# Kernel tuning notes

Measured on AMD Instinct MI355X. Metric: run time of the kernel, lower is better.

## Reference

```python
import jax, jax.numpy as jnp
import numpy as np

N = 8192
F_IN = 128
D = 128
NEG_SLOPE = 0.2  # cfg.negativeslope (standard GAT value)
MASK_FILL = -9e15


def setup_inputs() -> dict:
    key = jax.random.key(0)
    k1, k2, k3, k4 = jax.random.split(key, 4)
    A = jax.random.randint(k1, (N, N), 0, 2, dtype=jnp.int32)
    X = jax.random.normal(k2, (N, F_IN), dtype=jnp.float32)
    # glorot init for Ws, xavier_uniform(gain=1.414) for a
    lim_w = float(np.sqrt(6.0 / (F_IN + D)))
    Ws = jax.random.uniform(k3, (F_IN, D), minval=-lim_w, maxval=lim_w, dtype=jnp.float32)
    lim_a = 1.414 * float(np.sqrt(6.0 / (2 * D + 1)))
    a = jax.random.uniform(k4, (2 * D, 1), minval=-lim_a, maxval=lim_a, dtype=jnp.float32)
    return {"A": A, "X": X, "Ws": Ws, "a": a}


def reference(A, X, Ws, a):
    # Wh: [N, D]
    Wh = X @ Ws
    d = Wh.shape[-1]
    # additive attention: e_ij = leaky_relu(Wh_i . a1 + Wh_j . a2)
    e1 = Wh @ a[:d]          # [N, 1]
    e2 = Wh @ a[d:]          # [N, 1]
    e = jax.nn.leaky_relu(e1 + e2.T, negative_slope=NEG_SLOPE)  # [N, N]
    e = jnp.where(A > 0, e, MASK_FILL)
    attn = jax.nn.softmax(e, axis=1)  # row-wise over neighbors
    H = attn @ Wh            # [N, D]
    return H
```

## Files before the change

kernel.cpp:

```cpp
#include <hip/hip_runtime.h>
#include <hip/hip_bf16.h>

#define NN 8192
#define DD 128

typedef __attribute__((ext_vector_type(8))) short short8;
typedef __attribute__((ext_vector_type(4))) float f32x4;
typedef __attribute__((ext_vector_type(4))) int i32x4;
typedef unsigned int u32;
typedef unsigned long long u64;

__device__ __forceinline__ ushort f2bf(float f) {
    __hip_bfloat16 h = __float2bfloat16(f);
    return *(ushort*)&h;
}

__device__ __forceinline__ void async_ld16(const void* g, void* l) {
    __builtin_amdgcn_global_load_lds(
        (const __attribute__((address_space(1))) u32*)g,
        (__attribute__((address_space(3))) u32*)l, 16, 0, 0);
}

#define PACK4(b, v, sh)                                     \
    b |= (u32)((v).x & 1) << (sh);                          \
    b |= (u32)((v).y & 1) << ((sh) + 1);                    \
    b |= (u32)((v).z & 1) << ((sh) + 2);                    \
    b |= (u32)((v).w & 1) << ((sh) + 3);

__global__ __launch_bounds__(256) void k3a_pack(const int* __restrict__ A,
                                                uint4* __restrict__ Ap) {
    u32 T = blockIdx.x * 256 + threadIdx.x;
    u32 row = T >> 6, q = T & 63, kb = q >> 2, kg = q & 3;
    const int* base = A + (size_t)row * NN + kb * 512 + kg * 8;
    u32 d[4];
#pragma unroll
    for (int h = 0; h < 2; ++h) {
        i32x4 v[16];
#pragma unroll
        for (int j = 0; j < 8; ++j) {
            int kt = h * 4 + (j >> 1), tp = j & 1;
            const int* p = base + kt * 64 + tp * 32;
            v[j * 2]     = __builtin_nontemporal_load((const i32x4*)p);
            v[j * 2 + 1] = __builtin_nontemporal_load((const i32x4*)(p + 4));
        }
        u32 b01 = 0, b23 = 0;
#pragma unroll
        for (int j = 0; j < 8; ++j) {
            u32 b = 0;
            PACK4(b, v[j * 2], 0);
            PACK4(b, v[j * 2 + 1], 4);
            if (j < 4) b01 |= b << (8 * j);
            else       b23 |= b << (8 * (j - 4));
        }
        d[h * 2] = b01; d[h * 2 + 1] = b23;
    }
    Ap[T] = make_uint4(d[0], d[1], d[2], d[3]);
}

__global__ __launch_bounds__(256) void k12_gemm(const float* __restrict__ X,
                                                const float* __restrict__ Ws,
                                                const float* __restrict__ a,
                                                ushort* __restrict__ WhT,
                                                float* __restrict__ C1,
                                                float* __restrict__ C1s,
                                                float2* __restrict__ E2) {
    __shared__ float lWs[128 * 132];
    __shared__ float lX[32 * 132];
    __shared__ ushort lT2[128 * 32];
    __shared__ float la[256];
    int t = threadIdx.x, bx = blockIdx.x;
    la[t] = a[t];
    const float4* Ws4 = (const float4*)Ws;
    const float4* X4 = (const float4*)X;
    for (int j = 0; j < 16; ++j) {
        int u = j * 256 + t;
        int k = u >> 5, c4 = u & 31;
        *(float4*)&lWs[k * 132 + c4 * 4] = Ws4[u];
    }
    for (int j = 0; j < 4; ++j) {
        int u = j * 256 + t;
        int r = u >> 5, c4 = u & 31;
        *(float4*)&lX[r * 132 + c4 * 4] = X4[bx * 1024 + u];
    }
    __syncthreads();
    int r0 = (t >> 5) * 4, c0 = (t & 31) * 4;
    float acc[4][4];
#pragma unroll
    for (int i = 0; i < 4; ++i)
#pragma unroll
        for (int j = 0; j < 4; ++j) acc[i][j] = 0.f;
#pragma unroll 4
    for (int k = 0; k < 128; ++k) {
        float4 wv = *(const float4*)&lWs[k * 132 + c0];
        float x0 = lX[(r0 + 0) * 132 + k];
        float x1 = lX[(r0 + 1) * 132 + k];
        float x2 = lX[(r0 + 2) * 132 + k];
        float x3 = lX[(r0 + 3) * 132 + k];
#pragma unroll
        for (int j = 0; j < 4; ++j) {
            acc[0][j] += x0 * ((const float*)&wv)[j];
            acc[1][j] += x1 * ((const float*)&wv)[j];
            acc[2][j] += x2 * ((const float*)&wv)[j];
            acc[3][j] += x3 * ((const float*)&wv)[j];
        }
    }
#pragma unroll
    for (int i = 0; i < 4; ++i)
#pragma unroll
        for (int j = 0; j < 4; ++j)
            lT2[(c0 + j) * 32 + r0 + i] = f2bf(acc[i][j]);
    float p1[4], p2[4];
#pragma unroll
    for (int i = 0; i < 4; ++i) {
        p1[i] = 0.f; p2[i] = 0.f;
#pragma unroll
        for (int j = 0; j < 4; ++j) {
            p1[i] += acc[i][j] * la[c0 + j];
            p2[i] += acc[i][j] * la[128 + c0 + j];
        }
    }
#pragma unroll
    for (int m = 1; m < 32; m <<= 1) {
#pragma unroll
        for (int i = 0; i < 4; ++i) {
            p1[i] += __shfl_xor(p1[i], m);
            p2[i] += __shfl_xor(p2[i], m);
        }
    }
    if ((t & 31) == 0) {
#pragma unroll
        for (int i = 0; i < 4; ++i) {
            int row = bx * 32 + r0 + i;
            C1[row]  = __expf(p1[i]);
            C1s[row] = __expf(0.2f * p1[i]);
            E2[row]  = make_float2(__expf(p2[i]), __expf(0.2f * p2[i]));
        }
    }
    __syncthreads();
    {
        int d = t >> 1, hf = t & 1;
        uint4* dst = (uint4*)&WhT[(size_t)d * NN + bx * 32 + hf * 16];
        const uint4* src = (const uint4*)&lT2[d * 32 + hf * 16];
        dst[0] = src[0];
        dst[1] = src[1];
    }
}

__global__ __launch_bounds__(512, 2) void k3b_main(
    const uint4* __restrict__ Ap, const ushort* __restrict__ WhT,
    const float* __restrict__ C1, const float* __restrict__ C1s,
    const float2* __restrict__ E2,
    float* __restrict__ Hp, float* __restrict__ Lp) {

    __shared__ __align__(16) char lB[131072];
    __shared__ __align__(16) char lE[4096];

    int tid = threadIdx.x;
    int lane = tid & 63;
    int w = tid >> 6;
    int n = lane & 15;
    int kg = lane >> 4;

    int bx = blockIdx.x;
    int kb = blockIdx.y;
    int rb = bx * 256 + w * 32;

    float c1_0 = C1[rb + n],      c1s_0 = C1s[rb + n];
    float c1_1 = C1[rb + 16 + n], c1s_1 = C1s[rb + 16 + n];

    uint4 Mq0 = Ap[(size_t)(rb + n) * 64 + kb * 4 + kg];
    uint4 Mq1 = Ap[(size_t)(rb + 16 + n) * 64 + kb * 4 + kg];

#pragma unroll
    for (int i = 0; i < 16; ++i) {
        int p = w + i * 8;
        int kt = p >> 4, tp = (p >> 3) & 1, c = p & 7;
        const ushort* src = WhT + (size_t)(c * 16 + n) * NN +
                            (size_t)kb * 512 + kt * 64 + tp * 32 + kg * 8;
        async_ld16(src, lB + p * 1024 + lane * 16);
    }
    if (w == 0)
#pragma unroll
        for (int i = 0; i < 4; ++i)
            async_ld16((const char*)(E2 + (size_t)kb * 512) + (i * 64 + lane) * 16,
                       lE + (i * 64 + lane) * 16);

    short8 ones;
#pragma unroll
    for (int j = 0; j < 8; ++j) ones[j] = (short)0x3F80;

    f32x4 acc0[8], acc1[8];
#pragma unroll
    for (int c = 0; c < 8; ++c) {
        acc0[c] = (f32x4){0.f, 0.f, 0.f, 0.f};
        acc1[c] = (f32x4){0.f, 0.f, 0.f, 0.f};
    }
    f32x4 accl0 = (f32x4){0.f, 0.f, 0.f, 0.f};
    f32x4 accl1 = (f32x4){0.f, 0.f, 0.f, 0.f};

    __syncthreads();

#pragma unroll
    for (int kt = 0; kt < 8; ++kt) {
#pragma unroll
        for (int tp = 0; tp < 2; ++tp) {
            const int j = kt * 2 + tp;
            u32 d0 = (j < 4) ? Mq0.x : (j < 8) ? Mq0.y : (j < 12) ? Mq0.z : Mq0.w;
            u32 d1 = (j < 4) ? Mq1.x : (j < 8) ? Mq1.y : (j < 12) ? Mq1.z : Mq1.w;
            u32 ab0 = (d0 >> ((j & 3) * 8)) & 0xffu;
            u32 ab1 = (d1 >> ((j & 3) * 8)) & 0xffu;

            const float4* ev = (const float4*)((const float*)lE +
                                               (kt * 64 + tp * 32 + kg * 8) * 2);
            float pe[16];
            *(float4*)(pe + 0)  = ev[0];
            *(float4*)(pe + 4)  = ev[1];
            *(float4*)(pe + 8)  = ev[2];
            *(float4*)(pe + 12) = ev[3];
            short8 af0, af1;
#pragma unroll
            for (int u = 0; u < 8; ++u) {
                float w0 = fmaxf(c1_0 * pe[2 * u], c1s_0 * pe[2 * u + 1]);
                float w1 = fmaxf(c1_1 * pe[2 * u], c1s_1 * pe[2 * u + 1]);
                af0[u] = ((ab0 >> u) & 1u) ? (short)f2bf(w0) : (short)0;
                af1[u] = ((ab1 >> u) & 1u) ? (short)f2bf(w1) : (short)0;
            }
            const short8* bb = (const short8*)(lB + (kt * 16 + tp * 8) * 1024);
#pragma unroll
            for (int c = 0; c < 8; ++c) {
                short8 bf = bb[c * 64 + lane];
                acc0[c] = __builtin_amdgcn_mfma_f32_16x16x32_bf16(af0, bf, acc0[c], 0, 0, 0);
                acc1[c] = __builtin_amdgcn_mfma_f32_16x16x32_bf16(af1, bf, acc1[c], 0, 0, 0);
            }
            accl0 = __builtin_amdgcn_mfma_f32_16x16x32_bf16(af0, ones, accl0, 0, 0, 0);
            accl1 = __builtin_amdgcn_mfma_f32_16x16x32_bf16(af1, ones, accl1, 0, 0, 0);
        }
    }

    float* Hpb = Hp + (size_t)kb * (NN * DD);
#pragma unroll
    for (int c = 0; c < 8; ++c)
#pragma unroll
        for (int r = 0; r < 4; ++r) {
            Hpb[(size_t)(rb + kg * 4 + r) * DD + c * 16 + n]      = acc0[c][r];
            Hpb[(size_t)(rb + 16 + kg * 4 + r) * DD + c * 16 + n] = acc1[c][r];
        }
    if (n == 0) {
        float* Lpb = Lp + (size_t)kb * NN;
#pragma unroll
        for (int r = 0; r < 4; ++r) {
            Lpb[rb + kg * 4 + r]      = accl0[r];
            Lpb[rb + 16 + kg * 4 + r] = accl1[r];
        }
    }
}

__global__ void k4_final(const float* __restrict__ Hp, const float* __restrict__ Lp,
                         float* __restrict__ out) {
    int g = blockIdx.x * 256 + threadIdx.x;
    int i = g >> 5;
    float4 sv = make_float4(0.f, 0.f, 0.f, 0.f);
    float l = 0.f;
#pragma unroll
    for (int kb = 0; kb < 16; ++kb) {
        float4 v = *(const float4*)(Hp + (size_t)kb * (NN * DD) + (size_t)g * 4);
        sv.x += v.x; sv.y += v.y; sv.z += v.z; sv.w += v.w;
        l += Lp[(size_t)kb * NN + i];
    }
    float r = 1.f / l;
    *(float4*)(out + (size_t)g * 4) = make_float4(sv.x * r, sv.y * r, sv.z * r, sv.w * r);
}

extern "C" void kernel_launch(void* const* d_in, const int* in_sizes, int n_in,
                              void* d_out, int out_size, void* d_ws, size_t ws_size,
                              hipStream_t stream) {
    const int*   A  = (const int*)d_in[0];
    const float* X  = (const float*)d_in[1];
    const float* Ws = (const float*)d_in[2];
    const float* a  = (const float*)d_in[3];
    float* out = (float*)d_out;

    char* ws = (char*)d_ws;
    uint4*  Ap  = (uint4*)(ws);
    ushort* WhT = (ushort*)(ws + (8u << 20));
    float*  C1  = (float*)(ws + (10u << 20));
    float*  C1s = (float*)(ws + (10u << 20) + (32u << 10));
    float2* E2  = (float2*)(ws + (10u << 20) + (64u << 10));
    float*  Hp  = (float*)(ws + (11u << 20));
    float*  Lp  = (float*)(ws + (75u << 20));

    k3a_pack<<<2048, 256, 0, stream>>>(A, Ap);
    k12_gemm<<<256, 256, 0, stream>>>(X, Ws, a, WhT, C1, C1s, E2);
    k3b_main<<<dim3(32, 16), 512, 0, stream>>>(Ap, WhT, C1, C1s, E2, Hp, Lp);
    k4_final<<<1024, 256, 0, stream>>>(Hp, Lp, out);
}
```

Measured before the change: 411.1 us.

## Fuse pack and GEMM kernels; halve K-split in main attention kernel

```diff
diff --git a/kernel.cpp b/kernel.cpp
--- a/kernel.cpp
+++ b/kernel.cpp
@@ -27,37 +27,9 @@
     b |= (u32)((v).z & 1) << ((sh) + 2);                    \
     b |= (u32)((v).w & 1) << ((sh) + 3);
 
-__global__ __launch_bounds__(256) void k3a_pack(const int* __restrict__ A,
-                                                uint4* __restrict__ Ap) {
-    u32 T = blockIdx.x * 256 + threadIdx.x;
-    u32 row = T >> 6, q = T & 63, kb = q >> 2, kg = q & 3;
-    const int* base = A + (size_t)row * NN + kb * 512 + kg * 8;
-    u32 d[4];
-#pragma unroll
-    for (int h = 0; h < 2; ++h) {
-        i32x4 v[16];
-#pragma unroll
-        for (int j = 0; j < 8; ++j) {
-            int kt = h * 4 + (j >> 1), tp = j & 1;
-            const int* p = base + kt * 64 + tp * 32;
-            v[j * 2]     = __builtin_nontemporal_load((const i32x4*)p);
-            v[j * 2 + 1] = __builtin_nontemporal_load((const i32x4*)(p + 4));
-        }
-        u32 b01 = 0, b23 = 0;
-#pragma unroll
-        for (int j = 0; j < 8; ++j) {
-            u32 b = 0;
-            PACK4(b, v[j * 2], 0);
-            PACK4(b, v[j * 2 + 1], 4);
-            if (j < 4) b01 |= b << (8 * j);
-            else       b23 |= b << (8 * (j - 4));
-        }
-        d[h * 2] = b01; d[h * 2 + 1] = b23;
-    }
-    Ap[T] = make_uint4(d[0], d[1], d[2], d[3]);
-}
-
-__global__ __launch_bounds__(256) void k12_gemm(const float* __restrict__ X,
+__global__ __launch_bounds__(256) void kA_fused(const int* __restrict__ A,
+                                                uint4* __restrict__ Ap,
+                                                const float* __restrict__ X,
                                                 const float* __restrict__ Ws,
                                                 const float* __restrict__ a,
                                                 ushort* __restrict__ WhT,
@@ -68,7 +40,41 @@
     __shared__ float lX[32 * 132];
     __shared__ ushort lT2[128 * 32];
     __shared__ float la[256];
-    int t = threadIdx.x, bx = blockIdx.x;
+    int t = threadIdx.x;
+    int bxr = blockIdx.x;
+
+    if (bxr % 9 != 0) {
+        u32 p = bxr - bxr / 9 - 1;
+        u32 T = p * 256 + t;
+        u32 row = T >> 6, q = T & 63, kb = q >> 2, kg = q & 3;
+        const int* base = A + (size_t)row * NN + kb * 512 + kg * 8;
+        u32 d[4];
+#pragma unroll
+        for (int h = 0; h < 2; ++h) {
+            i32x4 v[16];
+#pragma unroll
+            for (int j = 0; j < 8; ++j) {
+                int kt = h * 4 + (j >> 1), tp = j & 1;
+                const int* pp = base + kt * 64 + tp * 32;
+                v[j * 2]     = __builtin_nontemporal_load((const i32x4*)pp);
+                v[j * 2 + 1] = __builtin_nontemporal_load((const i32x4*)(pp + 4));
+            }
+            u32 b01 = 0, b23 = 0;
+#pragma unroll
+            for (int j = 0; j < 8; ++j) {
+                u32 b = 0;
+                PACK4(b, v[j * 2], 0);
+                PACK4(b, v[j * 2 + 1], 4);
+                if (j < 4) b01 |= b << (8 * j);
+                else       b23 |= b << (8 * (j - 4));
+            }
+            d[h * 2] = b01; d[h * 2 + 1] = b23;
+        }
+        Ap[T] = make_uint4(d[0], d[1], d[2], d[3]);
+        return;
+    }
+
+    int bx = bxr / 9;
     la[t] = a[t];
     const float4* Ws4 = (const float4*)Ws;
     const float4* X4 = (const float4*)X;
@@ -153,7 +159,7 @@
     float* __restrict__ Hp, float* __restrict__ Lp) {
 
     __shared__ __align__(16) char lB[131072];
-    __shared__ __align__(16) char lE[4096];
+    __shared__ __align__(16) char lE[8192];
 
     int tid = threadIdx.x;
     int lane = tid & 63;
@@ -168,21 +174,25 @@
     float c1_0 = C1[rb + n],      c1s_0 = C1s[rb + n];
     float c1_1 = C1[rb + 16 + n], c1s_1 = C1s[rb + 16 + n];
 
-    uint4 Mq0 = Ap[(size_t)(rb + n) * 64 + kb * 4 + kg];
-    uint4 Mq1 = Ap[(size_t)(rb + 16 + n) * 64 + kb * 4 + kg];
+    uint4 Mq0[2], Mq1[2];
+#pragma unroll
+    for (int h = 0; h < 2; ++h) {
+        Mq0[h] = Ap[(size_t)(rb + n) * 64 + (kb * 2 + h) * 4 + kg];
+        Mq1[h] = Ap[(size_t)(rb + 16 + n) * 64 + (kb * 2 + h) * 4 + kg];
+    }
 
 #pragma unroll
     for (int i = 0; i < 16; ++i) {
         int p = w + i * 8;
         int kt = p >> 4, tp = (p >> 3) & 1, c = p & 7;
         const ushort* src = WhT + (size_t)(c * 16 + n) * NN +
-                            (size_t)kb * 512 + kt * 64 + tp * 32 + kg * 8;
+                            (size_t)kb * 1024 + kt * 64 + tp * 32 + kg * 8;
         async_ld16(src, lB + p * 1024 + lane * 16);
     }
     if (w == 0)
 #pragma unroll
-        for (int i = 0; i < 4; ++i)
-            async_ld16((const char*)(E2 + (size_t)kb * 512) + (i * 64 + lane) * 16,
+        for (int i = 0; i < 8; ++i)
+            async_ld16((const char*)(E2 + (size_t)kb * 1024) + (i * 64 + lane) * 16,
                        lE + (i * 64 + lane) * 16);
 
     short8 ones;
@@ -201,39 +211,54 @@
     __syncthreads();
 
 #pragma unroll
-    for (int kt = 0; kt < 8; ++kt) {
-#pragma unroll
-        for (int tp = 0; tp < 2; ++tp) {
-            const int j = kt * 2 + tp;
-            u32 d0 = (j < 4) ? Mq0.x : (j < 8) ? Mq0.y : (j < 12) ? Mq0.z : Mq0.w;
-            u32 d1 = (j < 4) ? Mq1.x : (j < 8) ? Mq1.y : (j < 12) ? Mq1.z : Mq1.w;
-            u32 ab0 = (d0 >> ((j & 3) * 8)) & 0xffu;
-            u32 ab1 = (d1 >> ((j & 3) * 8)) & 0xffu;
-
-            const float4* ev = (const float4*)((const float*)lE +
-                                               (kt * 64 + tp * 32 + kg * 8) * 2);
-            float pe[16];
-            *(float4*)(pe + 0)  = ev[0];
-            *(float4*)(pe + 4)  = ev[1];
-            *(float4*)(pe + 8)  = ev[2];
-            *(float4*)(pe + 12) = ev[3];
-            short8 af0, af1;
-#pragma unroll
-            for (int u = 0; u < 8; ++u) {
-                float w0 = fmaxf(c1_0 * pe[2 * u], c1s_0 * pe[2 * u + 1]);
-                float w1 = fmaxf(c1_1 * pe[2 * u], c1s_1 * pe[2 * u + 1]);
-                af0[u] = ((ab0 >> u) & 1u) ? (short)f2bf(w0) : (short)0;
-                af1[u] = ((ab1 >> u) & 1u) ? (short)f2bf(w1) : (short)0;
+    for (int h = 0; h < 2; ++h) {
+        if (h == 1) {
+            __syncthreads();
+#pragma unroll
+            for (int i = 0; i < 16; ++i) {
+                int p = w + i * 8;
+                int kt = p >> 4, tp = (p >> 3) & 1, c = p & 7;
+                const ushort* src = WhT + (size_t)(c * 16 + n) * NN +
+                                    (size_t)kb * 1024 + 512 + kt * 64 + tp * 32 + kg * 8;
+                async_ld16(src, lB + p * 1024 + lane * 16);
             }
-            const short8* bb = (const short8*)(lB + (kt * 16 + tp * 8) * 1024);
-#pragma unroll
-            for (int c = 0; c < 8; ++c) {
-                short8 bf = bb[c * 64 + lane];
-                acc0[c] = __builtin_amdgcn_mfma_f32_16x16x32_bf16(af0, bf, acc0[c], 0, 0, 0);
-                acc1[c] = __builtin_amdgcn_mfma_f32_16x16x32_bf16(af1, bf, acc1[c], 0, 0, 0);
+            __syncthreads();
+        }
+#pragma unroll
+        for (int kt = 0; kt < 8; ++kt) {
+#pragma unroll
+            for (int tp = 0; tp < 2; ++tp) {
+                const int j = kt * 2 + tp;
+                u32 d0 = (j < 4) ? Mq0[h].x : (j < 8) ? Mq0[h].y : (j < 12) ? Mq0[h].z : Mq0[h].w;
+                u32 d1 = (j < 4) ? Mq1[h].x : (j < 8) ? Mq1[h].y : (j < 12) ? Mq1[h].z : Mq1[h].w;
+                u32 ab0 = (d0 >> ((j & 3) * 8)) & 0xffu;
+                u32 ab1 = (d1 >> ((j & 3) * 8)) & 0xffu;
+
+                const float4* ev = (const float4*)((const float*)lE +
+                                                   (h * 512 + kt * 64 + tp * 32 + kg * 8) * 2);
+                float pe[16];
+                *(float4*)(pe + 0)  = ev[0];
+                *(float4*)(pe + 4)  = ev[1];
+                *(float4*)(pe + 8)  = ev[2];
+                *(float4*)(pe + 12) = ev[3];
+                short8 af0, af1;
+#pragma unroll
+                for (int u = 0; u < 8; ++u) {
+                    float w0 = fmaxf(c1_0 * pe[2 * u], c1s_0 * pe[2 * u + 1]);
+                    float w1 = fmaxf(c1_1 * pe[2 * u], c1s_1 * pe[2 * u + 1]);
+                    af0[u] = ((ab0 >> u) & 1u) ? (short)f2bf(w0) : (short)0;
+                    af1[u] = ((ab1 >> u) & 1u) ? (short)f2bf(w1) : (short)0;
+                }
+                const short8* bb = (const short8*)(lB + (kt * 16 + tp * 8) * 1024);
+#pragma unroll
+                for (int c = 0; c < 8; ++c) {
+                    short8 bf = bb[c * 64 + lane];
+                    acc0[c] = __builtin_amdgcn_mfma_f32_16x16x32_bf16(af0, bf, acc0[c], 0, 0, 0);
+                    acc1[c] = __builtin_amdgcn_mfma_f32_16x16x32_bf16(af1, bf, acc1[c], 0, 0, 0);
+                }
+                accl0 = __builtin_amdgcn_mfma_f32_16x16x32_bf16(af0, ones, accl0, 0, 0, 0);
+                accl1 = __builtin_amdgcn_mfma_f32_16x16x32_bf16(af1, ones, accl1, 0, 0, 0);
             }
-            accl0 = __builtin_amdgcn_mfma_f32_16x16x32_bf16(af0, ones, accl0, 0, 0, 0);
-            accl1 = __builtin_amdgcn_mfma_f32_16x16x32_bf16(af1, ones, accl1, 0, 0, 0);
         }
     }
 
@@ -262,7 +287,7 @@
     float4 sv = make_float4(0.f, 0.f, 0.f, 0.f);
     float l = 0.f;
 #pragma unroll
-    for (int kb = 0; kb < 16; ++kb) {
+    for (int kb = 0; kb < 8; ++kb) {
         float4 v = *(const float4*)(Hp + (size_t)kb * (NN * DD) + (size_t)g * 4);
         sv.x += v.x; sv.y += v.y; sv.z += v.z; sv.w += v.w;
         l += Lp[(size_t)kb * NN + i];
@@ -287,10 +312,9 @@
     float*  C1s = (float*)(ws + (10u << 20) + (32u << 10));
     float2* E2  = (float2*)(ws + (10u << 20) + (64u << 10));
     float*  Hp  = (float*)(ws + (11u << 20));
-    float*  Lp  = (float*)(ws + (75u << 20));
-
-    k3a_pack<<<2048, 256, 0, stream>>>(A, Ap);
-    k12_gemm<<<256, 256, 0, stream>>>(X, Ws, a, WhT, C1, C1s, E2);
-    k3b_main<<<dim3(32, 16), 512, 0, stream>>>(Ap, WhT, C1, C1s, E2, Hp, Lp);
+    float*  Lp  = (float*)(ws + (43u << 20));
+
+    kA_fused<<<2304, 256, 0, stream>>>(A, Ap, X, Ws, a, WhT, C1, C1s, E2);
+    k3b_main<<<dim3(32, 8), 512, 0, stream>>>(Ap, WhT, C1, C1s, E2, Hp, Lp);
     k4_final<<<1024, 256, 0, stream>>>(Hp, Lp, out);
 }
```

Result: no change. 409.4 us (-0.4%).
